# Optimization experiments

Measured on AMD Instinct MI355X. Metric: run time of the kernel, lower is better.

Reference implementation:

```python
import jax, jax.numpy as jnp
import numpy as np

B, S, DIM = 4, 2048, 512
HEADS, DHEAD = 8, 64
INNER = HEADS * DHEAD


def setup_inputs() -> dict:
    key = jax.random.key(0)
    k1, k2, k3, k4 = jax.random.split(key, 4)
    x = jax.random.normal(k1, (B, S, DIM), dtype=jnp.float32)
    W_qkv = jax.random.normal(k2, (DIM, 3 * INNER), dtype=jnp.float32) * (DIM ** -0.5)
    W_out = jax.random.normal(k3, (INNER, DIM), dtype=jnp.float32) * (INNER ** -0.5)
    b_out = jnp.zeros((DIM,), dtype=jnp.float32)
    # learnable log-temperature, initialized to log(dim_head**-0.5)
    log_temp = jnp.asarray(np.log(DHEAD ** -0.5), dtype=jnp.float32)
    return {"x": x, "W_qkv": W_qkv, "log_temp": log_temp, "W_out": W_out, "b_out": b_out}


def reference(x, W_qkv, log_temp, W_out, b_out):
    b, s, _ = x.shape
    qkv = x @ W_qkv  # [b, s, 3*inner]
    q, k, v = jnp.split(qkv, 3, axis=-1)
    # [b, s, inner] -> [b, h, s, d]
    reshape = lambda t: t.reshape(b, s, HEADS, DHEAD).transpose(0, 2, 1, 3)
    q, k, v = reshape(q), reshape(k), reshape(v)
    dots = jnp.einsum("bhid,bhjd->bhij", q, k) * jnp.exp(log_temp)
    mask_value = -jnp.finfo(dots.dtype).max
    eye = jnp.eye(s, dtype=bool)
    dots = jnp.where(eye, mask_value, dots)
    attn = jax.nn.softmax(dots, axis=-1)
    out = jnp.einsum("bhij,bhjd->bhid", attn, v)
    out = out.transpose(0, 2, 1, 3).reshape(b, s, INNER)
    return out @ W_out + b_out
```

## Files before the change

### kernel.cpp

```cpp
#include <hip/hip_runtime.h>
#include <hip/hip_bf16.h>

#define BB 4
#define SS 2048
#define DIMM 512
#define HH 8
#define DD 64
#define NQKV 1536

typedef float  floatx4 __attribute__((ext_vector_type(4)));
typedef short  bf16x8  __attribute__((ext_vector_type(8)));
typedef short  bf16x4  __attribute__((ext_vector_type(4)));

#define MFMA16(A, B, C) __builtin_amdgcn_mfma_f32_16x16x32_bf16(A, B, C, 0, 0, 0)

__device__ __forceinline__ unsigned short f2bf(float f) {
    unsigned int u = __float_as_uint(f);
    u += 0x7FFFu + ((u >> 16) & 1u);
    return (unsigned short)(u >> 16);
}

__device__ __forceinline__ unsigned int cvtpk(float lo, float hi) {
    unsigned int r;
    asm("v_cvt_pk_bf16_f32 %0, %1, %2" : "=v"(r) : "v"(lo), "v"(hi));
    return r;
}

__device__ __forceinline__ float fast_exp2(float x) {
#if __has_builtin(__builtin_amdgcn_exp2f)
    return __builtin_amdgcn_exp2f(x);
#else
    return __exp2f(x);
#endif
}

__device__ __forceinline__ void gl_lds16(const void* g, void* l) {
    __builtin_amdgcn_global_load_lds(
        (__attribute__((address_space(1))) void*)g,
        (__attribute__((address_space(3))) void*)l,
        16, 0, 0);
}

__global__ __launch_bounds__(256) void k_prep(
    const float* __restrict__ x, const float* __restrict__ W_qkv,
    const float* __restrict__ W_out,
    unsigned short* __restrict__ xb, unsigned short* __restrict__ Wq_t,
    unsigned short* __restrict__ Wo_t) {
    __shared__ float t[32][33];
    int bid = blockIdx.x, tid = threadIdx.x;
    if (bid < 4096) {
        int i = (bid * 256 + tid) * 4;
        float4 v = *(const float4*)(x + i);
        ushort4 o;
        o.x = f2bf(v.x); o.y = f2bf(v.y); o.z = f2bf(v.z); o.w = f2bf(v.w);
        *(ushort4*)(xb + i) = o;
        return;
    }
    const float* in; unsigned short* out; int R = 512, C, bx, by;
    if (bid < 4864) { in = W_qkv; out = Wq_t; C = 1536; int blk = bid - 4096; bx = blk % 48; by = blk / 48; }
    else            { in = W_out; out = Wo_t; C = 512;  int blk = bid - 4864; bx = blk % 16; by = blk / 16; }
    int tx = tid & 31, ty = tid >> 5;
    int c0 = bx * 32, r0 = by * 32;
    for (int i = 0; i < 4; i++) {
        int r = r0 + ty + i * 8;
        t[ty + i * 8][tx] = in[(size_t)r * C + c0 + tx];
    }
    __syncthreads();
    for (int i = 0; i < 4; i++) {
        int cc = c0 + ty + i * 8;
        out[(size_t)cc * R + r0 + tx] = f2bf(t[tx][ty + i * 8]);
    }
}

__global__ __launch_bounds__(256) void k_gemm_qkv(
    const unsigned short* __restrict__ A,
    const unsigned short* __restrict__ Bt,
    const float* __restrict__ log_temp,
    unsigned short* __restrict__ Qb,
    unsigned short* __restrict__ Kb,
    unsigned short* __restrict__ Vt) {
    __shared__ unsigned short smem[2][128 * 64];
    unsigned short* As = smem[0];
    unsigned short* Bs = smem[1];
    const int K = 512;
    int m0 = blockIdx.x * 128, n0 = blockIdx.y * 128;
    int tid = threadIdx.x;
    int w = tid >> 6, lane = tid & 63;
    int c = lane & 15, q4 = lane >> 4;
    int wm = w >> 1, wn = w & 1;
    float qscale = __expf(log_temp[0]) * 1.44269504f;

    floatx4 acc[4][4] = {};

    for (int k0 = 0; k0 < K; k0 += 64) {
        __syncthreads();
        for (int i = 0; i < 4; i++) {
            int cidx = w * 256 + i * 64 + lane;
            int row = cidx >> 3, cc = cidx & 7;
            int gcc = cc ^ (row & 7);
            gl_lds16(A + (size_t)(m0 + row) * K + k0 + gcc * 8,
                     As + (size_t)(w * 256 + i * 64) * 8);
            gl_lds16(Bt + (size_t)(n0 + row) * K + k0 + gcc * 8,
                     Bs + (size_t)(w * 256 + i * 64) * 8);
        }
        __syncthreads();
        bf16x8 aF[2][4], bF[2][4];
        for (int kh = 0; kh < 2; kh++)
            for (int mt = 0; mt < 4; mt++) {
                int row = wm * 64 + mt * 16 + c;
                aF[kh][mt] = *(const bf16x8*)&As[row * 64 + (((kh * 4 + q4) ^ (row & 7)) * 8)];
            }
        for (int kh = 0; kh < 2; kh++)
            for (int nt = 0; nt < 4; nt++) {
                int row = wn * 64 + nt * 16 + c;
                bF[kh][nt] = *(const bf16x8*)&Bs[row * 64 + (((kh * 4 + q4) ^ (row & 7)) * 8)];
            }
        for (int kh = 0; kh < 2; kh++)
            for (int mt = 0; mt < 4; mt++)
                for (int nt = 0; nt < 4; nt++)
                    acc[mt][nt] = MFMA16(aF[kh][mt], bF[kh][nt], acc[mt][nt]);
    }

    if (n0 < 1024) {
        for (int nt = 0; nt < 4; nt++) {
            int n = n0 + wn * 64 + nt * 16 + c;
            int t = n >> 9, inner = n & 511;
            int h = inner >> 6, d = inner & 63;
            for (int mt = 0; mt < 4; mt++) {
                for (int r = 0; r < 4; r++) {
                    int m = m0 + wm * 64 + mt * 16 + q4 * 4 + r;
                    int b = m >> 11, s = m & 2047;
                    int bh = b * 8 + h;
                    float v = acc[mt][nt][r];
                    if (t == 0)  Qb[((size_t)bh * SS + s) * 64 + d] = f2bf(v * qscale);
                    else         Kb[((size_t)bh * SS + s) * 64 + d] = f2bf(v);
                }
            }
        }
    } else {
        unsigned short* T = &smem[0][0];
        int b = m0 >> 11, s_base = m0 & 2047;
        for (int half = 0; half < 2; half++) {
            __syncthreads();
            if (wn == half) {
                for (int nt = 0; nt < 4; nt++)
                    for (int mt = 0; mt < 4; mt++)
                        for (int r = 0; r < 4; r++)
                            T[(nt * 16 + c) * 136 + wm * 64 + mt * 16 + q4 * 4 + r] =
                                f2bf(acc[mt][nt][r]);
            }
            __syncthreads();
            for (int rr = 0; rr < 4; rr++) {
                int nl = w * 16 + rr * 4 + q4;
                int ml = c * 8;
                bf16x8 v = *(const bf16x8*)&T[nl * 136 + ml];
                int n = n0 + half * 64 + nl;
                int h = (n >> 6) - 16, d = n & 63;
                int bh = b * 8 + h;
                *(bf16x8*)(Vt + ((size_t)bh * 64 + d) * SS + s_base + ml) = v;
            }
        }
    }
}

__global__ __launch_bounds__(512, 4) void k_attn(
    const unsigned short* __restrict__ Qb,
    const unsigned short* __restrict__ Kb,
    const unsigned short* __restrict__ Vt,
    unsigned short* __restrict__ AO) {
    __shared__ unsigned short KVs[2][2][2][64 * 64];
    int bid = blockIdx.x;
    int swz = (bid & 7) * 64 + (bid >> 3);
    int q0 = (swz & 15) * 128;
    int bh = swz >> 4;
    int h = bh & 7, b = bh >> 3;
    int tid = threadIdx.x, w = tid >> 6, lane = tid & 63;
    int wg = w >> 2, wi = w & 3;
    int c = lane & 15, q4 = lane >> 4;

    const unsigned short* Kbase = Kb + (size_t)bh * SS * 64 + (size_t)wg * 1024 * 64;
    const unsigned short* Vbase = Vt + (size_t)bh * 64 * SS;

    bf16x8 qf[2][2];
    for (int mt = 0; mt < 2; mt++) {
        const unsigned short* qp = Qb + ((size_t)bh * SS + q0 + wi * 32 + mt * 16 + c) * 64;
        qf[mt][0] = *(const bf16x8*)(qp + q4 * 8);
        qf[mt][1] = *(const bf16x8*)(qp + 32 + q4 * 8);
    }
    bf16x8 ones;
    for (int i = 0; i < 8; i++) ones[i] = (short)0x3F80;
    const floatx4 fzero = {};

    int cidx0 = wi * 128 + lane, cidx1 = cidx0 + 64;
    int row0 = cidx0 >> 3, cc0 = cidx0 & 7;
    int row1 = cidx1 >> 3, cc1 = cidx1 & 7;
    int fk0 = (row0 & 3) | ((row0 >> 1) & 4);
    int fk1 = (row1 & 3) | ((row1 >> 1) & 4);
    const unsigned short* ksrc0 = Kbase + (size_t)row0 * 64 + (cc0 ^ fk0) * 8;
    const unsigned short* ksrc1 = Kbase + (size_t)row1 * 64 + (cc1 ^ fk1) * 8;
    const unsigned short* vsrc0 = Vbase + (size_t)row0 * SS + wg * 1024 + (cc0 ^ (row0 & 7)) * 8;
    const unsigned short* vsrc1 = Vbase + (size_t)row1 * SS + wg * 1024 + (cc1 ^ (row1 & 7)) * 8;
    unsigned short* kdst0 = &KVs[0][wg][0][0] + wi * 1024;
    unsigned short* kdst1 = kdst0 + 512;
    unsigned short* vdst0 = &KVs[1][wg][0][0] + wi * 1024;
    unsigned short* vdst1 = vdst0 + 512;

    gl_lds16(ksrc0, kdst0); gl_lds16(ksrc1, kdst1);
    gl_lds16(vsrc0, vdst0); gl_lds16(vsrc1, vdst1);

    int mask_j0 = (q0 + wi * 32) & ~63;
    int mglob0 = q0 + wi * 32 + c;
    int mglob1 = mglob0 + 16;
    floatx4 oacc[2][4] = {};
    floatx4 osum[2] = {};

    for (int jt = 0; jt < 16; jt++) {
        int buf = jt & 1;
        int j0 = wg * 1024 + jt * 64;
        __syncthreads();
        if (jt + 1 < 16) {
            int jl = (jt + 1) * 64;
            gl_lds16(ksrc0 + (size_t)jl * 64, kdst0 + (buf ^ 1) * 4096);
            gl_lds16(ksrc1 + (size_t)jl * 64, kdst1 + (buf ^ 1) * 4096);
            gl_lds16(vsrc0 + jl, vdst0 + (buf ^ 1) * 4096);
            gl_lds16(vsrc1 + jl, vdst1 + (buf ^ 1) * 4096);
        }
        const unsigned short* Ksb = &KVs[0][wg][buf][0];
        const unsigned short* Vsb = &KVs[1][wg][buf][0];

        floatx4 sa[2][2][2];
        for (int g = 0; g < 2; g++) {
            bf16x8 kf[2][2];
            for (int inner = 0; inner < 2; inner++) {
                int row = g * 32 + ((c >> 2) << 3) + inner * 4 + (c & 3);
                kf[inner][0] = *(const bf16x8*)&Ksb[row * 64 + ((q4 ^ (c & 7)) * 8)];
                kf[inner][1] = *(const bf16x8*)&Ksb[row * 64 + (((4 + q4) ^ (c & 7)) * 8)];
            }
            __builtin_amdgcn_s_setprio(1);
            for (int mt = 0; mt < 2; mt++)
                for (int inner = 0; inner < 2; inner++) {
                    floatx4 t = MFMA16(kf[inner][0], qf[mt][0], fzero);
                    t = MFMA16(kf[inner][1], qf[mt][1], t);
                    sa[g][mt][inner] = t;
                }
            __builtin_amdgcn_s_setprio(0);
        }

        if (j0 == mask_j0) {
            for (int g = 0; g < 2; g++)
                for (int inner = 0; inner < 2; inner++)
                    for (int r = 0; r < 4; r++) {
                        int jg = j0 + g * 32 + q4 * 8 + inner * 4 + r;
                        if (jg == mglob0) sa[g][0][inner][r] = -1e30f;
                        if (jg == mglob1) sa[g][1][inner][r] = -1e30f;
                    }
        }

        for (int g = 0; g < 2; g++) {
            bf16x8 vf[4];
            for (int dt = 0; dt < 4; dt++) {
                int vrow = dt * 16 + c;
                vf[dt] = *(const bf16x8*)&Vsb[vrow * 64 + (((g * 4 + q4) ^ (c & 7)) * 8)];
            }
            for (int mt = 0; mt < 2; mt++) {
                float e0 = fast_exp2(sa[g][mt][0][0]), e1 = fast_exp2(sa[g][mt][0][1]);
                float e2 = fast_exp2(sa[g][mt][0][2]), e3 = fast_exp2(sa[g][mt][0][3]);
                float e4 = fast_exp2(sa[g][mt][1][0]), e5 = fast_exp2(sa[g][mt][1][1]);
                float e6 = fast_exp2(sa[g][mt][1][2]), e7 = fast_exp2(sa[g][mt][1][3]);
                union { bf16x8 v; unsigned int u[4]; } P;
                P.u[0] = cvtpk(e0, e1); P.u[1] = cvtpk(e2, e3);
                P.u[2] = cvtpk(e4, e5); P.u[3] = cvtpk(e6, e7);
                __builtin_amdgcn_s_setprio(1);
                for (int dt = 0; dt < 4; dt++)
                    oacc[mt][dt] = MFMA16(P.v, vf[dt], oacc[mt][dt]);
                osum[mt] = MFMA16(P.v, ones, osum[mt]);
                __builtin_amdgcn_s_setprio(0);
            }
        }
    }

    __syncthreads();
    float* p = (float*)&KVs[0][0][0][0] + ((size_t)(wi * 64 + lane)) * 41;
    if (wg == 1) {
        for (int mt = 0; mt < 2; mt++)
            for (int dt = 0; dt < 4; dt++)
                for (int r = 0; r < 4; r++)
                    p[mt * 16 + dt * 4 + r] = oacc[mt][dt][r];
        for (int mt = 0; mt < 2; mt++)
            for (int r = 0; r < 4; r++)
                p[32 + mt * 4 + r] = osum[mt][r];
    }
    __syncthreads();
    if (wg == 0) {
        for (int mt = 0; mt < 2; mt++)
            for (int dt = 0; dt < 4; dt++)
                for (int r = 0; r < 4; r++)
                    oacc[mt][dt][r] += p[mt * 16 + dt * 4 + r];
        for (int mt = 0; mt < 2; mt++)
            for (int r = 0; r < 4; r++)
                osum[mt][r] += p[32 + mt * 4 + r];

        for (int mt = 0; mt < 2; mt++) {
            for (int r = 0; r < 4; r++) {
                float inv = 1.0f / osum[mt][r];
                int s = q0 + wi * 32 + mt * 16 + q4 * 4 + r;
                for (int dt = 0; dt < 4; dt++)
                    AO[((size_t)b * SS + s) * 512 + h * 64 + dt * 16 + c] =
                        f2bf(oacc[mt][dt][r] * inv);
            }
        }
    }
}

__global__ __launch_bounds__(256) void k_gemm_out(
    const unsigned short* __restrict__ A,
    const unsigned short* __restrict__ Bt,
    const float* __restrict__ bias,
    float* __restrict__ out) {
    __shared__ unsigned short As[64 * 64];
    __shared__ unsigned short Bs[128 * 64];
    const int K = 512;
    int m0 = blockIdx.x * 64, n0 = blockIdx.y * 128;
    int tid = threadIdx.x;
    int w = tid >> 6, lane = tid & 63;
    int c = lane & 15, q4 = lane >> 4;

    floatx4 acc[8] = {};

    for (int k0 = 0; k0 < K; k0 += 64) {
        __syncthreads();
        for (int i = 0; i < 2; i++) {
            int cidx = i * 256 + tid;
            int row = cidx >> 3, cc = cidx & 7;
            int gcc = cc ^ (row & 7);
            gl_lds16(A + (size_t)(m0 + row) * K + k0 + gcc * 8,
                     As + (size_t)(i * 256 + w * 64) * 8);
        }
        for (int i = 0; i < 4; i++) {
            int cidx = i * 256 + tid;
            int row = cidx >> 3, cc = cidx & 7;
            int gcc = cc ^ (row & 7);
            gl_lds16(Bt + (size_t)(n0 + row) * K + k0 + gcc * 8,
                     Bs + (size_t)(i * 256 + w * 64) * 8);
        }
        __syncthreads();
        bf16x8 aF[2], bF[2][8];
        for (int kh = 0; kh < 2; kh++) {
            int row = w * 16 + c;
            aF[kh] = *(const bf16x8*)&As[row * 64 + (((kh * 4 + q4) ^ (row & 7)) * 8)];
        }
        for (int kh = 0; kh < 2; kh++)
            for (int nt = 0; nt < 8; nt++) {
                int row = nt * 16 + c;
                bF[kh][nt] = *(const bf16x8*)&Bs[row * 64 + (((kh * 4 + q4) ^ (row & 7)) * 8)];
            }
        for (int kh = 0; kh < 2; kh++)
            for (int nt = 0; nt < 8; nt++)
                acc[nt] = MFMA16(aF[kh], bF[kh][nt], acc[nt]);
    }

    for (int nt = 0; nt < 8; nt++) {
        int n = n0 + nt * 16 + c;
        float bv = bias[n];
        for (int r = 0; r < 4; r++) {
            int m = m0 + w * 16 + q4 * 4 + r;
            out[(size_t)m * 512 + n] = acc[nt][r] + bv;
        }
    }
}

extern "C" void kernel_launch(void* const* d_in, const int* in_sizes, int n_in,
                              void* d_out, int out_size, void* d_ws, size_t ws_size,
                              hipStream_t stream) {
    const float* x        = (const float*)d_in[0];
    const float* W_qkv    = (const float*)d_in[1];
    const float* log_temp = (const float*)d_in[2];
    const float* W_out    = (const float*)d_in[3];
    const float* b_out    = (const float*)d_in[4];
    float* out = (float*)d_out;

    char* ws = (char*)d_ws;
    unsigned short* xb   = (unsigned short*)(ws + 0);
    unsigned short* Wq_t = (unsigned short*)(ws + 8388608);
    unsigned short* Wo_t = (unsigned short*)(ws + 9961472);
    unsigned short* Qb   = (unsigned short*)(ws + 10485760);
    unsigned short* Kb   = (unsigned short*)(ws + 18874368);
    unsigned short* Vt   = (unsigned short*)(ws + 27262976);
    unsigned short* AO   = (unsigned short*)(ws + 35651584);

    k_prep<<<5120, 256, 0, stream>>>(x, W_qkv, W_out, xb, Wq_t, Wo_t);
    k_gemm_qkv<<<dim3(64, 12), 256, 0, stream>>>(xb, Wq_t, log_temp, Qb, Kb, Vt);
    k_attn<<<512, 512, 0, stream>>>(Qb, Kb, Vt, AO);
    k_gemm_out<<<dim3(128, 4), 256, 0, stream>>>(AO, Wo_t, b_out, out);
}
```

Before: 143.3 us.

## Fuse x bf16 conversion into QKV GEMM with double-buffered B and smaller out tiles

The separate fp32-to-bf16 conversion pass over x is removed. The QKV GEMM now loads fp32 x straight into registers, converts and stores it to LDS, and prefetches the next A tile and a double-buffered B tile while the current tile's MFMAs run. The output GEMM tile shrinks to 64x64 with more blocks and an occupancy hint. This drops one launch and a write plus read of xb, but the QKV GEMM reads twice the A bytes (12 column blocks each re-read the fp32 x) and gains register pressure and extra barriers.

```diff
diff --git a/kernel.cpp b/kernel.cpp
--- a/kernel.cpp
+++ b/kernel.cpp
@@ -42,23 +42,13 @@
 }
 
 __global__ __launch_bounds__(256) void k_prep(
-    const float* __restrict__ x, const float* __restrict__ W_qkv,
-    const float* __restrict__ W_out,
-    unsigned short* __restrict__ xb, unsigned short* __restrict__ Wq_t,
-    unsigned short* __restrict__ Wo_t) {
+    const float* __restrict__ W_qkv, const float* __restrict__ W_out,
+    unsigned short* __restrict__ Wq_t, unsigned short* __restrict__ Wo_t) {
     __shared__ float t[32][33];
     int bid = blockIdx.x, tid = threadIdx.x;
-    if (bid < 4096) {
-        int i = (bid * 256 + tid) * 4;
-        float4 v = *(const float4*)(x + i);
-        ushort4 o;
-        o.x = f2bf(v.x); o.y = f2bf(v.y); o.z = f2bf(v.z); o.w = f2bf(v.w);
-        *(ushort4*)(xb + i) = o;
-        return;
-    }
     const float* in; unsigned short* out; int R = 512, C, bx, by;
-    if (bid < 4864) { in = W_qkv; out = Wq_t; C = 1536; int blk = bid - 4096; bx = blk % 48; by = blk / 48; }
-    else            { in = W_out; out = Wo_t; C = 512;  int blk = bid - 4864; bx = blk % 16; by = blk / 16; }
+    if (bid < 768) { in = W_qkv; out = Wq_t; C = 1536; bx = bid % 48; by = bid / 48; }
+    else           { in = W_out; out = Wo_t; C = 512;  int blk = bid - 768; bx = blk % 16; by = blk / 16; }
     int tx = tid & 31, ty = tid >> 5;
     int c0 = bx * 32, r0 = by * 32;
     for (int i = 0; i < 4; i++) {
@@ -72,16 +62,15 @@
     }
 }
 
-__global__ __launch_bounds__(256) void k_gemm_qkv(
-    const unsigned short* __restrict__ A,
+__global__ __launch_bounds__(256, 3) void k_gemm_qkv(
+    const float* __restrict__ X,
     const unsigned short* __restrict__ Bt,
     const float* __restrict__ log_temp,
     unsigned short* __restrict__ Qb,
     unsigned short* __restrict__ Kb,
     unsigned short* __restrict__ Vt) {
-    __shared__ unsigned short smem[2][128 * 64];
-    unsigned short* As = smem[0];
-    unsigned short* Bs = smem[1];
+    __shared__ __align__(16) unsigned short smem[3 * 8192];
+    unsigned short* As = smem;
     const int K = 512;
     int m0 = blockIdx.x * 128, n0 = blockIdx.y * 128;
     int tid = threadIdx.x;
@@ -90,35 +79,66 @@
     int wm = w >> 1, wn = w & 1;
     float qscale = __expf(log_temp[0]) * 1.44269504f;
 
-    floatx4 acc[4][4] = {};
-
-    for (int k0 = 0; k0 < K; k0 += 64) {
-        __syncthreads();
+    int arow[4], agcc[4];
+    for (int j = 0; j < 4; j++) {
+        int cidx = w * 256 + j * 64 + lane;
+        arow[j] = cidx >> 3;
+        agcc[j] = (cidx & 7) ^ (arow[j] & 7);
+    }
+    floatx4 a0[4], a1[4];
+
+    auto load_A = [&](int k0) {
+        for (int j = 0; j < 4; j++) {
+            const float* p = X + (size_t)(m0 + arow[j]) * K + k0 + agcc[j] * 8;
+            a0[j] = *(const floatx4*)p;
+            a1[j] = *(const floatx4*)(p + 4);
+        }
+    };
+    auto issue_B = [&](int k0, int bsel) {
+        unsigned short* Bdst = smem + 8192 + bsel * 8192;
         for (int i = 0; i < 4; i++) {
             int cidx = w * 256 + i * 64 + lane;
             int row = cidx >> 3, cc = cidx & 7;
             int gcc = cc ^ (row & 7);
-            gl_lds16(A + (size_t)(m0 + row) * K + k0 + gcc * 8,
-                     As + (size_t)(w * 256 + i * 64) * 8);
             gl_lds16(Bt + (size_t)(n0 + row) * K + k0 + gcc * 8,
-                     Bs + (size_t)(w * 256 + i * 64) * 8);
-        }
+                     Bdst + (size_t)(w * 256 + i * 64) * 8);
+        }
+    };
+
+    floatx4 acc[4][4] = {};
+    load_A(0);
+    issue_B(0, 0);
+    int bsel = 0;
+
+    for (int k0 = 0; k0 < K; k0 += 64) {
         __syncthreads();
-        bf16x8 aF[2][4], bF[2][4];
-        for (int kh = 0; kh < 2; kh++)
+        for (int j = 0; j < 4; j++) {
+            union { bf16x8 v; unsigned int u[4]; } t;
+            t.u[0] = cvtpk(a0[j][0], a0[j][1]);
+            t.u[1] = cvtpk(a0[j][2], a0[j][3]);
+            t.u[2] = cvtpk(a1[j][0], a1[j][1]);
+            t.u[3] = cvtpk(a1[j][2], a1[j][3]);
+            *(bf16x8*)&As[(size_t)(w * 256 + j * 64 + lane) * 8] = t.v;
+        }
+        __syncthreads();
+        if (k0 + 64 < K) { issue_B(k0 + 64, bsel ^ 1); load_A(k0 + 64); }
+
+        const unsigned short* Bcur = smem + 8192 + bsel * 8192;
+        for (int kh = 0; kh < 2; kh++) {
+            bf16x8 aF[4], bF[4];
             for (int mt = 0; mt < 4; mt++) {
                 int row = wm * 64 + mt * 16 + c;
-                aF[kh][mt] = *(const bf16x8*)&As[row * 64 + (((kh * 4 + q4) ^ (row & 7)) * 8)];
-            }
-        for (int kh = 0; kh < 2; kh++)
+                aF[mt] = *(const bf16x8*)&As[row * 64 + (((kh * 4 + q4) ^ (row & 7)) * 8)];
+            }
             for (int nt = 0; nt < 4; nt++) {
                 int row = wn * 64 + nt * 16 + c;
-                bF[kh][nt] = *(const bf16x8*)&Bs[row * 64 + (((kh * 4 + q4) ^ (row & 7)) * 8)];
-            }
-        for (int kh = 0; kh < 2; kh++)
+                bF[nt] = *(const bf16x8*)&Bcur[row * 64 + (((kh * 4 + q4) ^ (row & 7)) * 8)];
+            }
             for (int mt = 0; mt < 4; mt++)
                 for (int nt = 0; nt < 4; nt++)
-                    acc[mt][nt] = MFMA16(aF[kh][mt], bF[kh][nt], acc[mt][nt]);
+                    acc[mt][nt] = MFMA16(aF[mt], bF[nt], acc[mt][nt]);
+        }
+        bsel ^= 1;
     }
 
     if (n0 < 1024) {
@@ -138,7 +158,7 @@
             }
         }
     } else {
-        unsigned short* T = &smem[0][0];
+        unsigned short* T = smem;
         int b = m0 >> 11, s_base = m0 & 2047;
         for (int half = 0; half < 2; half++) {
             __syncthreads();
@@ -312,20 +332,20 @@
     }
 }
 
-__global__ __launch_bounds__(256) void k_gemm_out(
+__global__ __launch_bounds__(256, 4) void k_gemm_out(
     const unsigned short* __restrict__ A,
     const unsigned short* __restrict__ Bt,
     const float* __restrict__ bias,
     float* __restrict__ out) {
     __shared__ unsigned short As[64 * 64];
-    __shared__ unsigned short Bs[128 * 64];
+    __shared__ unsigned short Bs[64 * 64];
     const int K = 512;
-    int m0 = blockIdx.x * 64, n0 = blockIdx.y * 128;
+    int m0 = blockIdx.x * 64, n0 = blockIdx.y * 64;
     int tid = threadIdx.x;
     int w = tid >> 6, lane = tid & 63;
     int c = lane & 15, q4 = lane >> 4;
 
-    floatx4 acc[8] = {};
+    floatx4 acc[4] = {};
 
     for (int k0 = 0; k0 < K; k0 += 64) {
         __syncthreads();
@@ -335,31 +355,24 @@
             int gcc = cc ^ (row & 7);
             gl_lds16(A + (size_t)(m0 + row) * K + k0 + gcc * 8,
                      As + (size_t)(i * 256 + w * 64) * 8);
-        }
-        for (int i = 0; i < 4; i++) {
-            int cidx = i * 256 + tid;
-            int row = cidx >> 3, cc = cidx & 7;
-            int gcc = cc ^ (row & 7);
             gl_lds16(Bt + (size_t)(n0 + row) * K + k0 + gcc * 8,
                      Bs + (size_t)(i * 256 + w * 64) * 8);
         }
         __syncthreads();
-        bf16x8 aF[2], bF[2][8];
         for (int kh = 0; kh < 2; kh++) {
             int row = w * 16 + c;
-            aF[kh] = *(const bf16x8*)&As[row * 64 + (((kh * 4 + q4) ^ (row & 7)) * 8)];
-        }
-        for (int kh = 0; kh < 2; kh++)
-            for (int nt = 0; nt < 8; nt++) {
-                int row = nt * 16 + c;
-                bF[kh][nt] = *(const bf16x8*)&Bs[row * 64 + (((kh * 4 + q4) ^ (row & 7)) * 8)];
-            }
-        for (int kh = 0; kh < 2; kh++)
-            for (int nt = 0; nt < 8; nt++)
-                acc[nt] = MFMA16(aF[kh], bF[kh][nt], acc[nt]);
-    }
-
-    for (int nt = 0; nt < 8; nt++) {
+            bf16x8 aF = *(const bf16x8*)&As[row * 64 + (((kh * 4 + q4) ^ (row & 7)) * 8)];
+            bf16x8 bF[4];
+            for (int nt = 0; nt < 4; nt++) {
+                int rown = nt * 16 + c;
+                bF[nt] = *(const bf16x8*)&Bs[rown * 64 + (((kh * 4 + q4) ^ (rown & 7)) * 8)];
+            }
+            for (int nt = 0; nt < 4; nt++)
+                acc[nt] = MFMA16(aF, bF[nt], acc[nt]);
+        }
+    }
+
+    for (int nt = 0; nt < 4; nt++) {
         int n = n0 + nt * 16 + c;
         float bv = bias[n];
         for (int r = 0; r < 4; r++) {
@@ -380,7 +393,6 @@
     float* out = (float*)d_out;
 
     char* ws = (char*)d_ws;
-    unsigned short* xb   = (unsigned short*)(ws + 0);
     unsigned short* Wq_t = (unsigned short*)(ws + 8388608);
     unsigned short* Wo_t = (unsigned short*)(ws + 9961472);
     unsigned short* Qb   = (unsigned short*)(ws + 10485760);
@@ -388,8 +400,8 @@
     unsigned short* Vt   = (unsigned short*)(ws + 27262976);
     unsigned short* AO   = (unsigned short*)(ws + 35651584);
 
-    k_prep<<<5120, 256, 0, stream>>>(x, W_qkv, W_out, xb, Wq_t, Wo_t);
-    k_gemm_qkv<<<dim3(64, 12), 256, 0, stream>>>(xb, Wq_t, log_temp, Qb, Kb, Vt);
+    k_prep<<<1024, 256, 0, stream>>>(W_qkv, W_out, Wq_t, Wo_t);
+    k_gemm_qkv<<<dim3(64, 12), 256, 0, stream>>>(x, Wq_t, log_temp, Qb, Kb, Vt);
     k_attn<<<512, 512, 0, stream>>>(Qb, Kb, Vt, AO);
-    k_gemm_out<<<dim3(128, 4), 256, 0, stream>>>(AO, Wo_t, b_out, out);
-}
+    k_gemm_out<<<dim3(128, 8), 256, 0, stream>>>(AO, Wo_t, b_out, out);
+}
```

Measured after the change: 139.8 us (median of 2 runs). -2.4%, faster.
